# Kernel tuning notes

Hardware: AMD Instinct MI355X
Metric: run time of the kernel (lower is better)

## Reference

```python
import jax, jax.numpy as jnp
import numpy as np

NS = 16384   # N*S support examples
NQ = 16384   # N*Q query examples
D = 64       # embedding dim
N_CLASSES = 64


def setup_inputs() -> dict:
    key = jax.random.key(0)
    k1, k2, k3 = jax.random.split(key, 3)
    support_embeddings = jax.random.normal(k1, (NS, D), dtype=jnp.float32)
    query_embeddings = jax.random.normal(k2, (NQ, D), dtype=jnp.float32)
    labels = jax.random.randint(k3, (NS,), 0, N_CLASSES)
    support_labels_onehot = jax.nn.one_hot(labels, N_CLASSES, dtype=jnp.float32)
    return {
        "support_embeddings": support_embeddings,
        "query_embeddings": query_embeddings,
        "support_labels_onehot": support_labels_onehot,
    }


def reference(support_embeddings, query_embeddings, support_labels_onehot):
    # Pairwise L2 distance via ||q||^2 + ||s||^2 - 2 q.s (same math as
    # tf.norm(q[:,None,:] - s[None,:,:], axis=2) without the [NQ,NS,D] blowup).
    sq_s = jnp.sum(support_embeddings * support_embeddings, axis=-1)  # [NS]
    sq_q = jnp.sum(query_embeddings * query_embeddings, axis=-1)      # [NQ]
    cross = jnp.einsum('qd,sd->qs', query_embeddings, support_embeddings)  # [NQ,NS]
    d2 = sq_q[:, None] + sq_s[None, :] - 2.0 * cross
    distance = jnp.sqrt(jnp.maximum(d2, 0.0))
    # top_k(-distance, k=1) == first argmin along support axis
    indices = jnp.argmin(distance, axis=1)                 # [NQ]
    labels_x = jnp.argmax(support_labels_onehot, axis=1)   # [NS]
    labels_pred = labels_x[indices]                        # [NQ] gather
    num_classes = support_labels_onehot.shape[1]
    labels_prob = jax.nn.one_hot(labels_pred, num_classes, dtype=support_labels_onehot.dtype)
    return labels_prob
```

## Files before the change

### kernel.cpp

```cpp
#include <hip/hip_runtime.h>


#define NTOT   16384
#define DIM    64
#define EPS_COEF 0.004f
#define EPS_ABS  0.05f
#define CINIT_COEF (-0.499f)
#define FLT_BIG 3.4e38f

typedef __attribute__((ext_vector_type(8))) short short8;
typedef __attribute__((ext_vector_type(4))) float float4v;

__device__ __forceinline__ ushort f16_bits(float x) {
  union { _Float16 f; ushort u; } c;
  c.f = (_Float16)x;
  return c.u;
}

__device__ __forceinline__ void pin8(short8& v) {
  asm volatile("" : "+v"(v));
}

__global__ __launch_bounds__(256) void k_prep(
    const float* __restrict__ S, const float* __restrict__ Q,
    ushort* __restrict__ Sh, ushort* __restrict__ Qh,
    float* __restrict__ sqS, float* __restrict__ sqQ,
    float* __restrict__ S_T) {
  __shared__ float tile[64][65];
  const int tid = threadIdx.x;
  const bool isS = blockIdx.x < 256;
  const int rbase = (blockIdx.x & 255) * 64;
  const float* __restrict__ src = isS ? S : Q;
  ushort* __restrict__ dh = isS ? Sh : Qh;

  const int tx = tid & 63;
  const int ty = tid >> 6;
#pragma unroll
  for (int i = 0; i < 16; ++i) {
    const int r = i * 4 + ty;
    tile[r][tx] = src[(size_t)(rbase + r) * DIM + tx];
  }
  __syncthreads();

  if (isS) {
#pragma unroll
    for (int i = 0; i < 16; ++i) {
      const int d = i * 4 + ty;
      S_T[(size_t)d * NTOT + rbase + tx] = tile[tx][d];
    }
  }

  const int panel = tid >> 6;
  const int half = (tid >> 5) & 1;
  const int slot0 = (tid & 31) * 2;
#pragma unroll
  for (int ss = 0; ss < 2; ++ss) {
    const int s = slot0 + ss;
    const int m = s & 15;
    const int q8 = s >> 4;
    const int row = panel * 16 + m;
    const int kb = half * 32 + q8 * 8;
    short8 hv;
#pragma unroll
    for (int j = 0; j < 8; ++j) hv[j] = (short)f16_bits(tile[row][kb + j]);
    const size_t goff =
        (size_t)((rbase >> 4) + panel) * 1024 + (size_t)half * 512 + (size_t)s * 8;
    *(short8*)&dh[goff] = hv;
  }

  if (tid < 64) {
    float acc = 0.0f;
#pragma unroll
    for (int d = 0; d < DIM; ++d) {
      const float v = tile[tid][d];
      acc = fmaf(v, v, acc);
    }
    (isS ? sqS : sqQ)[rbase + tid] = acc;
  }
}


#define MFMA16F(A, B, C) __builtin_amdgcn_mfma_f32_16x16x32_f16(A, B, C, 0, 0, 0)

#define STEP_COMPUTE(H0, H1, SQ)                                           \
  do {                                                                     \
    float4v cinit;                                                         \
    cinit[0] = CINIT_COEF * SQ.x;                                          \
    cinit[1] = CINIT_COEF * SQ.y;                                          \
    cinit[2] = CINIT_COEF * SQ.z;                                          \
    cinit[3] = CINIT_COEF * SQ.w;                                          \
    _Pragma("unroll")                                                      \
    for (int t = 0; t < 4; ++t) {                                          \
      float4v a = MFMA16F(H0, qh[t][0], cinit);                            \
      a = MFMA16F(H1, qh[t][1], a);                                        \
      bmr[t] = fmaxf(bmr[t], fmaxf(fmaxf(a[0], a[1]), fmaxf(a[2], a[3]))); \
    }                                                                      \
  } while (0)

template <int BST>
__global__ __launch_bounds__(256, 3) void k_phaseA(
    const ushort* __restrict__ Sh, const ushort* __restrict__ Qh,
    const float* __restrict__ sqS, float* __restrict__ bmin) {
  constexpr int NSB = NTOT / (16 * BST);
  const int tid = threadIdx.x;
  const int l = tid & 63;
  const int w = tid >> 6;
  const int lm = l & 15;
  const int lq = l >> 4;
  const int split = blockIdx.x;
  const int qbase = blockIdx.y * 64;
  const int sbase = split * 2048 + w * 512;

  short8 qh[4][2];
#pragma unroll
  for (int t = 0; t < 4; ++t) {
    const size_t pb = (size_t)((qbase >> 4) + t) * 1024 + (size_t)l * 8;
    qh[t][0] = *(const short8*)&Qh[pb];
    qh[t][1] = *(const short8*)&Qh[pb + 512];
  }
#pragma unroll
  for (int t = 0; t < 4; ++t) {
    pin8(qh[t][0]);
    pin8(qh[t][1]);
  }

  const ushort* pSh = Sh + (size_t)(sbase >> 4) * 1024 + (size_t)l * 8;
  const float* psq = sqS + sbase + lq * 4;

  short8 h0a = *(const short8*)(pSh);
  short8 h1a = *(const short8*)(pSh + 512);
  float4 sqa = *(const float4*)(psq);
  short8 h0b = *(const short8*)(pSh + 1024);
  short8 h1b = *(const short8*)(pSh + 1024 + 512);
  float4 sqb = *(const float4*)(psq + 16);

  float bmr[4] = {-FLT_BIG, -FLT_BIG, -FLT_BIG, -FLT_BIG};

  for (int st = 0; st < 32; st += 2) {
    STEP_COMPUTE(h0a, h1a, sqa);
    if (st + 2 < 32) {
      const int off = (st + 2) * 1024;
      h0a = *(const short8*)(pSh + off);
      h1a = *(const short8*)(pSh + off + 512);
      sqa = *(const float4*)(psq + (st + 2) * 16);
    }
    STEP_COMPUTE(h0b, h1b, sqb);
    if (st + 3 < 32) {
      const int off = (st + 3) * 1024;
      h0b = *(const short8*)(pSh + off);
      h1b = *(const short8*)(pSh + off + 512);
      sqb = *(const float4*)(psq + (st + 3) * 16);
    }
    if (((st + 1) & (BST - 1)) == (BST - 1)) {
      const int gb = split * (128 / BST) + w * (32 / BST) + ((st + 1) / BST);
#pragma unroll
      for (int t = 0; t < 4; ++t) {
        float v = bmr[t];
        v = fmaxf(v, __shfl_xor(v, 16, 64));
        v = fmaxf(v, __shfl_xor(v, 32, 64));
        if (lq == 0) bmin[(size_t)(qbase + t * 16 + lm) * NSB + gb] = -2.0f * v;
        bmr[t] = -FLT_BIG;
      }
    }
  }
}

template <int SBLK>
__global__ __launch_bounds__(256) void k_phaseB(
    const float* __restrict__ S_T,
    const float* __restrict__ Q,
    const float* __restrict__ sqS, const float* __restrict__ sqQ,
    const float* __restrict__ bmin,
    const float* __restrict__ onehot, float* __restrict__ out) {
  constexpr int NSB = NTOT / SBLK;
  constexpr int NB64 = NSB / 64;
  constexpr int SPL = SBLK / 64;

  __shared__ float sQrow[4][64];
  const int lane = threadIdx.x & 63;
  const int w = threadIdx.x >> 6;
  const int q = blockIdx.x * 4 + w;

  if (lane < 16)
    *(float4*)&sQrow[w][lane * 4] = *(const float4*)&Q[(size_t)q * DIM + lane * 4];
  __syncthreads();

  const float eps = EPS_COEF * sqQ[q] + EPS_ABS;

  float bv[NB64];
#pragma unroll
  for (int j = 0; j < NB64; ++j) bv[j] = bmin[(size_t)q * NSB + j * 64 + lane];
  float m = bv[0];
#pragma unroll
  for (int j = 1; j < NB64; ++j) m = fminf(m, bv[j]);
#pragma unroll
  for (int d = 1; d < 64; d <<= 1) m = fminf(m, __shfl_xor(m, d, 64));
  const float thr = m + eps;

  float bk = FLT_BIG;
  int bi = 0;
#pragma unroll
  for (int j = 0; j < NB64; ++j) {
    unsigned long long msk = __ballot(bv[j] <= thr);
    while (msk) {
      const int b = j * 64 + (__ffsll((long long)msk) - 1);
      msk &= msk - 1;
      const int s0 = b * SBLK + lane * SPL;
      if (SPL == 2) {
        float a0 = 0.f, a1 = 0.f;
#pragma unroll
        for (int c = 0; c < 16; ++c) {
          const float4 qv = *(const float4*)&sQrow[w][c * 4];
          const float2 x0 = *(const float2*)&S_T[(size_t)(c * 4 + 0) * NTOT + s0];
          const float2 x1 = *(const float2*)&S_T[(size_t)(c * 4 + 1) * NTOT + s0];
          const float2 x2 = *(const float2*)&S_T[(size_t)(c * 4 + 2) * NTOT + s0];
          const float2 x3 = *(const float2*)&S_T[(size_t)(c * 4 + 3) * NTOT + s0];
          a0 = fmaf(qv.x, x0.x, a0); a1 = fmaf(qv.x, x0.y, a1);
          a0 = fmaf(qv.y, x1.x, a0); a1 = fmaf(qv.y, x1.y, a1);
          a0 = fmaf(qv.z, x2.x, a0); a1 = fmaf(qv.z, x2.y, a1);
          a0 = fmaf(qv.w, x3.x, a0); a1 = fmaf(qv.w, x3.y, a1);
        }
        const float2 sq2 = *(const float2*)&sqS[s0];
        const float k0 = fmaf(-2.f, a0, sq2.x);
        const float k1 = fmaf(-2.f, a1, sq2.y);
        bool u;
        u = k0 < bk; bk = u ? k0 : bk; bi = u ? s0 : bi;
        u = k1 < bk; bk = u ? k1 : bk; bi = u ? (s0 + 1) : bi;
      } else {
        float a0 = 0.f, a1 = 0.f, a2 = 0.f, a3 = 0.f;
#pragma unroll
        for (int c = 0; c < 16; ++c) {
          const float4 qv = *(const float4*)&sQrow[w][c * 4];
          const float4 s0v = *(const float4*)&S_T[(size_t)(c * 4 + 0) * NTOT + s0];
          const float4 s1v = *(const float4*)&S_T[(size_t)(c * 4 + 1) * NTOT + s0];
          const float4 s2v = *(const float4*)&S_T[(size_t)(c * 4 + 2) * NTOT + s0];
          const float4 s3v = *(const float4*)&S_T[(size_t)(c * 4 + 3) * NTOT + s0];
          a0 = fmaf(qv.x, s0v.x, a0); a1 = fmaf(qv.x, s0v.y, a1);
          a2 = fmaf(qv.x, s0v.z, a2); a3 = fmaf(qv.x, s0v.w, a3);
          a0 = fmaf(qv.y, s1v.x, a0); a1 = fmaf(qv.y, s1v.y, a1);
          a2 = fmaf(qv.y, s1v.z, a2); a3 = fmaf(qv.y, s1v.w, a3);
          a0 = fmaf(qv.z, s2v.x, a0); a1 = fmaf(qv.z, s2v.y, a1);
          a2 = fmaf(qv.z, s2v.z, a2); a3 = fmaf(qv.z, s2v.w, a3);
          a0 = fmaf(qv.w, s3v.x, a0); a1 = fmaf(qv.w, s3v.y, a1);
          a2 = fmaf(qv.w, s3v.z, a2); a3 = fmaf(qv.w, s3v.w, a3);
        }
        const float4 sq4 = *(const float4*)&sqS[s0];
        const float k0 = fmaf(-2.f, a0, sq4.x);
        const float k1 = fmaf(-2.f, a1, sq4.y);
        const float k2 = fmaf(-2.f, a2, sq4.z);
        const float k3 = fmaf(-2.f, a3, sq4.w);
        bool u;
        u = k0 < bk; bk = u ? k0 : bk; bi = u ? s0 : bi;
        u = k1 < bk; bk = u ? k1 : bk; bi = u ? (s0 + 1) : bi;
        u = k2 < bk; bk = u ? k2 : bk; bi = u ? (s0 + 2) : bi;
        u = k3 < bk; bk = u ? k3 : bk; bi = u ? (s0 + 3) : bi;
      }
    }
  }
#pragma unroll
  for (int d = 1; d < 64; d <<= 1) {
    const float ok = __shfl_xor(bk, d, 64);
    const int oi = __shfl_xor(bi, d, 64);
    const bool u = (ok < bk) || (ok == bk && oi < bi);
    bk = u ? ok : bk;
    bi = u ? oi : bi;
  }
  const float ov = onehot[(size_t)bi * 64 + lane];
  const unsigned long long lmask = __ballot(ov > 0.5f);
  const int label = __ffsll((long long)lmask) - 1;
  out[(size_t)q * 64 + lane] = (lane == label) ? 1.0f : 0.0f;
}

extern "C" void kernel_launch(void* const* d_in, const int* in_sizes, int n_in,
                              void* d_out, int out_size, void* d_ws, size_t ws_size,
                              hipStream_t stream) {
  const float* S = (const float*)d_in[0];
  const float* Q = (const float*)d_in[1];
  const float* OH = (const float*)d_in[2];
  float* out = (float*)d_out;

  char* ws = (char*)d_ws;
  ushort* Sh = (ushort*)ws;
  ushort* Qh = (ushort*)(ws + (2u << 20));
  float* S_T = (float*)(ws + (4u << 20));
  float* sqS = (float*)(ws + (8u << 20));
  float* sqQ = (float*)(ws + (8u << 20) + (64u << 10));
  float* bmin = (float*)(ws + (8u << 20) + (128u << 10));

  k_prep<<<dim3(512), 256, 0, stream>>>(S, Q, Sh, Qh, sqS, sqQ, S_T);

  if (ws_size >= (17u << 20)) {
    k_phaseA<8><<<dim3(8, NTOT / 64), 256, 0, stream>>>(Sh, Qh, sqS, bmin);
    k_phaseB<128><<<dim3(NTOT / 4), 256, 0, stream>>>(S_T, Q, sqS, sqQ,
                                                      bmin, OH, out);
  } else {
    k_phaseA<16><<<dim3(8, NTOT / 64), 256, 0, stream>>>(Sh, Qh, sqS, bmin);
    k_phaseB<256><<<dim3(NTOT / 4), 256, 0, stream>>>(S_T, Q, sqS, sqQ,
                                                      bmin, OH, out);
  }
  (void)in_sizes; (void)n_in; (void)out_size; (void)ws_size;
}
```

Before: 154.1 us.

## Balance phase-B candidate-block rescoring across the four waves of each block

Each wave no longer rescores only the candidate support blocks of its own query. The four queries' candidate masks go into shared memory and the combined candidate list is dealt round-robin across the four waves. Per-wave partial minima are then merged through shared memory. This targets load imbalance, where one query with many near-tie candidate blocks stalls the whole block, at the cost of an extra barrier, shared-memory traffic and per-query reduction loops.

```diff
diff --git a/kernel.cpp b/kernel.cpp
--- a/kernel.cpp
+++ b/kernel.cpp
@@ -177,13 +177,16 @@
   constexpr int SPL = SBLK / 64;
 
   __shared__ float sQrow[4][64];
+  __shared__ unsigned long long smask[4][NB64];
+  __shared__ float sbk[4][4];
+  __shared__ int sbi[4][4];
+
   const int lane = threadIdx.x & 63;
   const int w = threadIdx.x >> 6;
   const int q = blockIdx.x * 4 + w;
 
   if (lane < 16)
     *(float4*)&sQrow[w][lane * 4] = *(const float4*)&Q[(size_t)q * DIM + lane * 4];
-  __syncthreads();
 
   const float eps = EPS_COEF * sqQ[q] + EPS_ABS;
 
@@ -197,75 +200,99 @@
   for (int d = 1; d < 64; d <<= 1) m = fminf(m, __shfl_xor(m, d, 64));
   const float thr = m + eps;
 
-  float bk = FLT_BIG;
-  int bi = 0;
 #pragma unroll
   for (int j = 0; j < NB64; ++j) {
-    unsigned long long msk = __ballot(bv[j] <= thr);
-    while (msk) {
-      const int b = j * 64 + (__ffsll((long long)msk) - 1);
-      msk &= msk - 1;
-      const int s0 = b * SBLK + lane * SPL;
-      if (SPL == 2) {
-        float a0 = 0.f, a1 = 0.f;
-#pragma unroll
-        for (int c = 0; c < 16; ++c) {
-          const float4 qv = *(const float4*)&sQrow[w][c * 4];
-          const float2 x0 = *(const float2*)&S_T[(size_t)(c * 4 + 0) * NTOT + s0];
-          const float2 x1 = *(const float2*)&S_T[(size_t)(c * 4 + 1) * NTOT + s0];
-          const float2 x2 = *(const float2*)&S_T[(size_t)(c * 4 + 2) * NTOT + s0];
-          const float2 x3 = *(const float2*)&S_T[(size_t)(c * 4 + 3) * NTOT + s0];
-          a0 = fmaf(qv.x, x0.x, a0); a1 = fmaf(qv.x, x0.y, a1);
-          a0 = fmaf(qv.y, x1.x, a0); a1 = fmaf(qv.y, x1.y, a1);
-          a0 = fmaf(qv.z, x2.x, a0); a1 = fmaf(qv.z, x2.y, a1);
-          a0 = fmaf(qv.w, x3.x, a0); a1 = fmaf(qv.w, x3.y, a1);
+    const unsigned long long msk = __ballot(bv[j] <= thr);
+    if (lane == 0) smask[w][j] = msk;
+  }
+  __syncthreads();
+
+  int idx = 0;
+  for (int qq = 0; qq < 4; ++qq) {
+    float bkq = FLT_BIG;
+    int biq = 0;
+    for (int j = 0; j < NB64; ++j) {
+      unsigned long long msk = smask[qq][j];
+      while (msk) {
+        const int b = j * 64 + (__ffsll((long long)msk) - 1);
+        msk &= msk - 1;
+        if ((idx++ & 3) != w) continue;
+        const int s0 = b * SBLK + lane * SPL;
+        if (SPL == 2) {
+          float a0 = 0.f, a1 = 0.f;
+#pragma unroll
+          for (int c = 0; c < 16; ++c) {
+            const float4 qv = *(const float4*)&sQrow[qq][c * 4];
+            const float2 x0 = *(const float2*)&S_T[(size_t)(c * 4 + 0) * NTOT + s0];
+            const float2 x1 = *(const float2*)&S_T[(size_t)(c * 4 + 1) * NTOT + s0];
+            const float2 x2 = *(const float2*)&S_T[(size_t)(c * 4 + 2) * NTOT + s0];
+            const float2 x3 = *(const float2*)&S_T[(size_t)(c * 4 + 3) * NTOT + s0];
+            a0 = fmaf(qv.x, x0.x, a0); a1 = fmaf(qv.x, x0.y, a1);
+            a0 = fmaf(qv.y, x1.x, a0); a1 = fmaf(qv.y, x1.y, a1);
+            a0 = fmaf(qv.z, x2.x, a0); a1 = fmaf(qv.z, x2.y, a1);
+            a0 = fmaf(qv.w, x3.x, a0); a1 = fmaf(qv.w, x3.y, a1);
+          }
+          const float2 sq2 = *(const float2*)&sqS[s0];
+          const float k0 = fmaf(-2.f, a0, sq2.x);
+          const float k1 = fmaf(-2.f, a1, sq2.y);
+          bool u;
+          u = k0 < bkq; bkq = u ? k0 : bkq; biq = u ? s0 : biq;
+          u = k1 < bkq; bkq = u ? k1 : bkq; biq = u ? (s0 + 1) : biq;
+        } else {
+          float a0 = 0.f, a1 = 0.f, a2 = 0.f, a3 = 0.f;
+#pragma unroll
+          for (int c = 0; c < 16; ++c) {
+            const float4 qv = *(const float4*)&sQrow[qq][c * 4];
+            const float4 s0v = *(const float4*)&S_T[(size_t)(c * 4 + 0) * NTOT + s0];
+            const float4 s1v = *(const float4*)&S_T[(size_t)(c * 4 + 1) * NTOT + s0];
+            const float4 s2v = *(const float4*)&S_T[(size_t)(c * 4 + 2) * NTOT + s0];
+            const float4 s3v = *(const float4*)&S_T[(size_t)(c * 4 + 3) * NTOT + s0];
+            a0 = fmaf(qv.x, s0v.x, a0); a1 = fmaf(qv.x, s0v.y, a1);
+            a2 = fmaf(qv.x, s0v.z, a2); a3 = fmaf(qv.x, s0v.w, a3);
+            a0 = fmaf(qv.y, s1v.x, a0); a1 = fmaf(qv.y, s1v.y, a1);
+            a2 = fmaf(qv.y, s1v.z, a2); a3 = fmaf(qv.y, s1v.w, a3);
+            a0 = fmaf(qv.z, s2v.x, a0); a1 = fmaf(qv.z, s2v.y, a1);
+            a2 = fmaf(qv.z, s2v.z, a2); a3 = fmaf(qv.z, s2v.w, a3);
+            a0 = fmaf(qv.w, s3v.x, a0); a1 = fmaf(qv.w, s3v.y, a1);
+            a2 = fmaf(qv.w, s3v.z, a2); a3 = fmaf(qv.w, s3v.w, a3);
+          }
+          const float4 sq4 = *(const float4*)&sqS[s0];
+          const float k0 = fmaf(-2.f, a0, sq4.x);
+          const float k1 = fmaf(-2.f, a1, sq4.y);
+          const float k2 = fmaf(-2.f, a2, sq4.z);
+          const float k3 = fmaf(-2.f, a3, sq4.w);
+          bool u;
+          u = k0 < bkq; bkq = u ? k0 : bkq; biq = u ? s0 : biq;
+          u = k1 < bkq; bkq = u ? k1 : bkq; biq = u ? (s0 + 1) : biq;
+          u = k2 < bkq; bkq = u ? k2 : bkq; biq = u ? (s0 + 2) : biq;
+          u = k3 < bkq; bkq = u ? k3 : bkq; biq = u ? (s0 + 3) : biq;
         }
-        const float2 sq2 = *(const float2*)&sqS[s0];
-        const float k0 = fmaf(-2.f, a0, sq2.x);
-        const float k1 = fmaf(-2.f, a1, sq2.y);
-        bool u;
-        u = k0 < bk; bk = u ? k0 : bk; bi = u ? s0 : bi;
-        u = k1 < bk; bk = u ? k1 : bk; bi = u ? (s0 + 1) : bi;
-      } else {
-        float a0 = 0.f, a1 = 0.f, a2 = 0.f, a3 = 0.f;
-#pragma unroll
-        for (int c = 0; c < 16; ++c) {
-          const float4 qv = *(const float4*)&sQrow[w][c * 4];
-          const float4 s0v = *(const float4*)&S_T[(size_t)(c * 4 + 0) * NTOT + s0];
-          const float4 s1v = *(const float4*)&S_T[(size_t)(c * 4 + 1) * NTOT + s0];
-          const float4 s2v = *(const float4*)&S_T[(size_t)(c * 4 + 2) * NTOT + s0];
-          const float4 s3v = *(const float4*)&S_T[(size_t)(c * 4 + 3) * NTOT + s0];
-          a0 = fmaf(qv.x, s0v.x, a0); a1 = fmaf(qv.x, s0v.y, a1);
-          a2 = fmaf(qv.x, s0v.z, a2); a3 = fmaf(qv.x, s0v.w, a3);
-          a0 = fmaf(qv.y, s1v.x, a0); a1 = fmaf(qv.y, s1v.y, a1);
-          a2 = fmaf(qv.y, s1v.z, a2); a3 = fmaf(qv.y, s1v.w, a3);
-          a0 = fmaf(qv.z, s2v.x, a0); a1 = fmaf(qv.z, s2v.y, a1);
-          a2 = fmaf(qv.z, s2v.z, a2); a3 = fmaf(qv.z, s2v.w, a3);
-          a0 = fmaf(qv.w, s3v.x, a0); a1 = fmaf(qv.w, s3v.y, a1);
-          a2 = fmaf(qv.w, s3v.z, a2); a3 = fmaf(qv.w, s3v.w, a3);
-        }
-        const float4 sq4 = *(const float4*)&sqS[s0];
-        const float k0 = fmaf(-2.f, a0, sq4.x);
-        const float k1 = fmaf(-2.f, a1, sq4.y);
-        const float k2 = fmaf(-2.f, a2, sq4.z);
-        const float k3 = fmaf(-2.f, a3, sq4.w);
-        bool u;
-        u = k0 < bk; bk = u ? k0 : bk; bi = u ? s0 : bi;
-        u = k1 < bk; bk = u ? k1 : bk; bi = u ? (s0 + 1) : bi;
-        u = k2 < bk; bk = u ? k2 : bk; bi = u ? (s0 + 2) : bi;
-        u = k3 < bk; bk = u ? k3 : bk; bi = u ? (s0 + 3) : bi;
       }
     }
-  }
-#pragma unroll
-  for (int d = 1; d < 64; d <<= 1) {
-    const float ok = __shfl_xor(bk, d, 64);
-    const int oi = __shfl_xor(bi, d, 64);
-    const bool u = (ok < bk) || (ok == bk && oi < bi);
-    bk = u ? ok : bk;
-    bi = u ? oi : bi;
-  }
-  const float ov = onehot[(size_t)bi * 64 + lane];
+#pragma unroll
+    for (int d = 1; d < 64; d <<= 1) {
+      const float ok = __shfl_xor(bkq, d, 64);
+      const int oi = __shfl_xor(biq, d, 64);
+      const bool u = (ok < bkq) || (ok == bkq && oi < biq);
+      bkq = u ? ok : bkq;
+      biq = u ? oi : biq;
+    }
+    if (lane == 0) { sbk[qq][w] = bkq; sbi[qq][w] = biq; }
+  }
+  __syncthreads();
+
+  float fk = sbk[w][0];
+  int fi = sbi[w][0];
+#pragma unroll
+  for (int ww = 1; ww < 4; ++ww) {
+    const float ok = sbk[w][ww];
+    const int oi = sbi[w][ww];
+    const bool u = (ok < fk) || (ok == fk && oi < fi);
+    fk = u ? ok : fk;
+    fi = u ? oi : fi;
+  }
+
+  const float ov = onehot[(size_t)fi * 64 + lane];
   const unsigned long long lmask = __ballot(ov > 0.5f);
   const int label = __ffsll((long long)lmask) - 1;
   out[(size_t)q * 64 + lane] = (lane == label) ? 1.0f : 0.0f;
```

Result: no change. 153.0 us (-0.7%).
